# Kernel optimization log

Measured on AMD Instinct MI355X. Metric: run time of the kernel, lower is better.

Reference implementation:

```python
import jax, jax.numpy as jnp
import numpy as np

DIM = 192
NUM_HEADS = 6
WS = 7            # window_size
SS = 3            # shift_size
MLP_HIDDEN = int(DIM * 4.0)
HEAD_DIM = DIM // NUM_HEADS
SCALE = HEAD_DIM ** -0.5
N = WS * WS


def _relative_position_index(ws):
    coords = np.stack(np.meshgrid(np.arange(ws), np.arange(ws), indexing='ij'))  # [2,ws,ws]
    cf = coords.reshape(2, -1)
    rel = cf[:, :, None] - cf[:, None, :]          # [2,N,N]
    rel = rel.transpose(1, 2, 0).copy()
    rel[:, :, 0] += ws - 1
    rel[:, :, 1] += ws - 1
    rel[:, :, 0] *= 2 * ws - 1
    return rel.sum(-1)                              # [N,N]

RPI = jnp.asarray(_relative_position_index(WS))


def _attn_mask(Hp, Wp, ws, ss):
    img = np.zeros((Hp, Wp))
    cnt = 0
    slices = (slice(0, -ws), slice(-ws, -ss), slice(-ss, None))
    for h in slices:
        for w in slices:
            img[h, w] = cnt
            cnt += 1
    mw = img.reshape(Hp // ws, ws, Wp // ws, ws).transpose(0, 2, 1, 3).reshape(-1, ws * ws)
    am = mw[:, None, :] - mw[:, :, None]            # [nWins,N,N]
    am = np.where(am != 0, -100.0, 0.0).astype(np.float32)
    return jnp.asarray(am)


def _layernorm(x, g, b, eps=1e-5):
    mu = jnp.mean(x, axis=-1, keepdims=True)
    var = jnp.mean(jnp.square(x - mu), axis=-1, keepdims=True)
    return (x - mu) * jax.lax.rsqrt(var + eps) * g + b


def setup_inputs() -> dict:
    key = jax.random.key(0)
    ks = jax.random.split(key, 16)
    s = lambda k, shp, sc=0.02: jax.random.normal(k, shp, jnp.float32) * sc
    return {
        'x': jax.random.normal(ks[0], (32, 3136, DIM), jnp.float32),
        'qkv_w': s(ks[1], (DIM, 3 * DIM)),
        'qkv_b': jnp.zeros((3 * DIM,), jnp.float32),
        'proj_w': s(ks[2], (DIM, DIM)),
        'proj_b': jnp.zeros((DIM,), jnp.float32),
        'rpb_table': s(ks[3], ((2 * WS - 1) * (2 * WS - 1), NUM_HEADS)),
        'ln1_g': jnp.ones((DIM,), jnp.float32),
        'ln1_b': jnp.zeros((DIM,), jnp.float32),
        'ln2_g': jnp.ones((DIM,), jnp.float32),
        'ln2_b': jnp.zeros((DIM,), jnp.float32),
        'w1': s(ks[4], (DIM, MLP_HIDDEN)),
        'b1': jnp.zeros((MLP_HIDDEN,), jnp.float32),
        'w2': s(ks[5], (MLP_HIDDEN, DIM)),
        'b2': jnp.zeros((DIM,), jnp.float32),
        'H': 56,
        'W': 56,
    }


def reference(x, qkv_w, qkv_b, proj_w, proj_b, rpb_table, ln1_g, ln1_b,
              ln2_g, ln2_b, w1, b1, w2, b2, H, W):
    B, L, C = x.shape
    shortcut = x
    h = _layernorm(x, ln1_g, ln1_b).reshape(B, H, W, C)

    pad_r = (WS - W % WS) % WS
    pad_b = (WS - H % WS) % WS
    h = jnp.pad(h, ((0, 0), (0, pad_b), (0, pad_r), (0, 0)))
    Hp, Wp = H + pad_b, W + pad_r
    nH, nW = Hp // WS, Wp // WS
    nWins = nH * nW

    if SS > 0:
        h = jnp.roll(h, shift=(-SS, -SS), axis=(1, 2))
        attn_mask = _attn_mask(Hp, Wp, WS, SS)       # [nWins,N,N]
    else:
        attn_mask = None

    # window partition -> [B*nWins, N, C]
    win = h.reshape(B, nH, WS, nW, WS, C).transpose(0, 1, 3, 2, 4, 5)
    win = win.reshape(B * nWins, N, C)

    # attention
    qkv = win @ qkv_w + qkv_b                        # [B_,N,3C]
    qkv = qkv.reshape(-1, N, 3, NUM_HEADS, HEAD_DIM).transpose(2, 0, 3, 1, 4)
    q, k, v = qkv[0] * SCALE, qkv[1], qkv[2]         # [B_,h,N,d]
    attn = jnp.einsum('bhnd,bhmd->bhnm', q, k)

    rpb = rpb_table[RPI.reshape(-1)].reshape(N, N, NUM_HEADS).transpose(2, 0, 1)
    attn = attn + rpb[None]
    if attn_mask is not None:
        attn = attn.reshape(B, nWins, NUM_HEADS, N, N) + attn_mask[None, :, None]
        attn = attn.reshape(-1, NUM_HEADS, N, N)
    attn = jax.nn.softmax(attn, axis=-1)
    out = jnp.einsum('bhnm,bhmd->bhnd', attn, v).transpose(0, 2, 1, 3).reshape(-1, N, C)
    out = out @ proj_w + proj_b

    # window reverse
    out = out.reshape(B, nH, nW, WS, WS, C).transpose(0, 1, 3, 2, 4, 5).reshape(B, Hp, Wp, C)
    if SS > 0:
        out = jnp.roll(out, shift=(SS, SS), axis=(1, 2))
    if pad_r > 0 or pad_b > 0:
        out = out[:, :H, :W, :]
    out = out.reshape(B, H * W, C)

    h = shortcut + out
    ff = _layernorm(h, ln2_g, ln2_b)
    ff = jax.nn.gelu(ff @ w1 + b1, approximate=False) @ w2 + b2
    return h + ff
```

## Files before the change

### kernel.cpp

```cpp
#include <hip/hip_runtime.h>
#include <hip/hip_bf16.h>
#include <cstdint>

typedef __hip_bfloat16 bf16;
typedef __attribute__((ext_vector_type(4))) float f32x4;
typedef __attribute__((ext_vector_type(8))) __bf16 bf16x8;

#define SCALE 0.17677669529663687f

#define OFF_WTQ   0
#define OFF_WTP   221184
#define OFF_WT1   294912
#define OFF_WT2   589824
#define OFF_RMAP  884736
#define OFF_A     1286144
#define OFF_B     39821312
#define OFF_C     193961984

__global__ __launch_bounds__(256) void prep_k(
    const float* __restrict__ qkv_w, const float* __restrict__ proj_w,
    const float* __restrict__ w1, const float* __restrict__ w2,
    bf16* __restrict__ wtq, bf16* __restrict__ wtp,
    bf16* __restrict__ wt1, bf16* __restrict__ wt2, int* __restrict__ rmap)
{
  int i = blockIdx.x * 256 + threadIdx.x;
  if (i < 110592) {
    int n = i / 192, k = i - n * 192;
    wtq[i] = __float2bfloat16(qkv_w[k * 576 + n]);
  } else if (i < 147456) {
    int j = i - 110592; int n = j / 192, k = j - n * 192;
    wtp[j] = __float2bfloat16(proj_w[k * 192 + n]);
  } else if (i < 294912) {
    int j = i - 147456; int n = j / 192, k = j - n * 192;
    wt1[j] = __float2bfloat16(w1[k * 768 + n]);
  } else if (i < 442368) {
    int j = i - 294912; int n = j / 768, k = j - n * 768;
    wt2[j] = __float2bfloat16(w2[k * 192 + n]);
  } else if (i < 542720) {
    int m = i - 442368;
    int win = m / 49, nn = m - win * 49;
    int b = win >> 6, iw = win & 63;
    int wh = iw >> 3, ww = iw & 7;
    int ty = nn / 7, tx = nn - ty * 7;
    int rr = wh * 7 + ty + 3; if (rr >= 56) rr -= 56;
    int cc = ww * 7 + tx + 3; if (cc >= 56) cc -= 56;
    rmap[m] = b * 3136 + rr * 56 + cc;
  }
}

template<bool MAP>
__global__ __launch_bounds__(256) void ln_k(
    const float* __restrict__ x, const float* __restrict__ g,
    const float* __restrict__ b, const int* __restrict__ rmap,
    bf16* __restrict__ out)
{
  int wv = threadIdx.x >> 6, lane = threadIdx.x & 63;
  long m = (long)blockIdx.x * 4 + wv;
  long src = MAP ? (long)rmap[m] : m;
  const float* row = x + src * 192;
  float v0 = row[lane], v1 = row[lane + 64], v2 = row[lane + 128];
  float s = v0 + v1 + v2;
  #pragma unroll
  for (int d = 1; d < 64; d <<= 1) s += __shfl_xor(s, d, 64);
  float mu = s * (1.0f / 192.0f);
  float d0 = v0 - mu, d1 = v1 - mu, d2 = v2 - mu;
  float q = d0 * d0 + d1 * d1 + d2 * d2;
  #pragma unroll
  for (int d = 1; d < 64; d <<= 1) q += __shfl_xor(q, d, 64);
  float inv = 1.0f / sqrtf(q * (1.0f / 192.0f) + 1e-5f);
  bf16* o = out + m * 192;
  o[lane]       = __float2bfloat16(d0 * inv * g[lane]       + b[lane]);
  o[lane + 64]  = __float2bfloat16(d1 * inv * g[lane + 64]  + b[lane + 64]);
  o[lane + 128] = __float2bfloat16(d2 * inv * g[lane + 128] + b[lane + 128]);
}

template<int MODE, int KD>
__global__ __launch_bounds__(256) void gemm_k(
    const bf16* __restrict__ A, const bf16* __restrict__ Bt,
    const float* __restrict__ bias, const float* __restrict__ extra,
    const int* __restrict__ rmap, void* __restrict__ outp)
{
  __shared__ bf16 As[128 * 64];
  const int tid = threadIdx.x;
  const int lane = tid & 63;
  const int w = tid >> 6;
  const int wm = w >> 1, wn = w & 1;
  const long m0 = (long)blockIdx.y * 128;
  const int n0 = blockIdx.x * 64;
  const int r = lane & 15, kb = lane >> 4;

  f32x4 acc[4][2];
  #pragma unroll
  for (int a = 0; a < 4; ++a)
    #pragma unroll
    for (int bb = 0; bb < 2; ++bb) acc[a][bb] = (f32x4){0.f, 0.f, 0.f, 0.f};

  for (int k0 = 0; k0 < KD; k0 += 64) {
    #pragma unroll
    for (int it = 0; it < 4; ++it) {
      int li = tid + it * 256;
      int m = li >> 3;
      int sl = (li & 7) ^ (m & 7);
      const bf16* src = A + (m0 + m) * KD + k0 + sl * 8;
      bf16* dst = As + (size_t)(w * 64 + it * 256) * 8;
      __builtin_amdgcn_global_load_lds(
          (const __attribute__((address_space(1))) unsigned int*)src,
          (__attribute__((address_space(3))) unsigned int*)dst, 16, 0, 0);
    }
    __syncthreads();

    bf16x8 af[2][4], bfr[2][2];
    #pragma unroll
    for (int h2 = 0; h2 < 2; ++h2) {
      #pragma unroll
      for (int mi = 0; mi < 4; ++mi) {
        int m = wm * 64 + mi * 16 + r;
        int slot = (h2 * 4 + kb) ^ (r & 7);
        af[h2][mi] = *(const bf16x8*)(As + m * 64 + slot * 8);
      }
      #pragma unroll
      for (int ni = 0; ni < 2; ++ni) {
        int n = n0 + wn * 32 + ni * 16 + r;
        bfr[h2][ni] = *(const bf16x8*)(Bt + (long)n * KD + k0 + h2 * 32 + kb * 8);
      }
    }
    #pragma unroll
    for (int h2 = 0; h2 < 2; ++h2)
      #pragma unroll
      for (int mi = 0; mi < 4; ++mi)
        #pragma unroll
        for (int ni = 0; ni < 2; ++ni)
          acc[mi][ni] = __builtin_amdgcn_mfma_f32_16x16x32_bf16(
              af[h2][mi], bfr[h2][ni], acc[mi][ni], 0, 0, 0);
    __syncthreads();
  }

  #pragma unroll
  for (int mi = 0; mi < 4; ++mi) {
    #pragma unroll
    for (int ni = 0; ni < 2; ++ni) {
      int col = n0 + wn * 32 + ni * 16 + r;
      float bb = bias[col];
      #pragma unroll
      for (int rr = 0; rr < 4; ++rr) {
        long row = m0 + wm * 64 + mi * 16 + kb * 4 + rr;
        float c = acc[mi][ni][rr] + bb;
        if constexpr (MODE == 0) {
          ((bf16*)outp)[row * 576 + col] = __float2bfloat16(c);
        } else {
          long gr = rmap[row];
          ((float*)outp)[gr * 192 + col] = extra[gr * 192 + col] + c;
        }
      }
    }
  }
}

#define ALS 200
#define W1S 200
#define HLS 72
#define W2S 72
__global__ __launch_bounds__(512) void mlp_k(
    const float* __restrict__ h, const float* __restrict__ g2,
    const float* __restrict__ bg2, const bf16* __restrict__ w1t,
    const float* __restrict__ b1, const bf16* __restrict__ w2t,
    const float* __restrict__ b2, float* __restrict__ outp)
{
  __shared__ bf16 Al[128 * ALS];
  __shared__ bf16 W1c[64 * W1S];
  __shared__ bf16 Hl[128 * HLS];
  __shared__ bf16 W2c[192 * W2S];
  const int tid = threadIdx.x;
  const int lane = tid & 63, w = tid >> 6;
  const int wm = w >> 1, wn = w & 1;
  const int r = lane & 15, kb = lane >> 4;
  const long m0 = (long)blockIdx.x * 128;

  bf16x8 wst[6];
  #pragma unroll
  for (int j = 0; j < 3; ++j) {
    int uu = j * 512 + tid;
    int row = uu / 24, sl = uu - row * 24;
    wst[j] = *(const bf16x8*)(w1t + row * 192 + sl * 8);
  }
  #pragma unroll
  for (int j = 0; j < 3; ++j) {
    int uu = j * 512 + tid;
    int row = uu >> 3, sl = uu & 7;
    wst[3 + j] = *(const bf16x8*)(w2t + row * 768 + sl * 8);
  }

  {
    float gv0 = g2[lane], gv1 = g2[lane + 64], gv2 = g2[lane + 128];
    float bv0 = bg2[lane], bv1 = bg2[lane + 64], bv2 = bg2[lane + 128];
    #pragma unroll
    for (int half = 0; half < 2; ++half) {
      float va[8][3];
      #pragma unroll
      for (int i = 0; i < 8; ++i) {
        const float* row = h + (m0 + w * 16 + half * 8 + i) * 192;
        va[i][0] = row[lane]; va[i][1] = row[lane + 64]; va[i][2] = row[lane + 128];
      }
      #pragma unroll
      for (int i = 0; i < 8; ++i) {
        float s = va[i][0] + va[i][1] + va[i][2];
        #pragma unroll
        for (int d = 1; d < 64; d <<= 1) s += __shfl_xor(s, d, 64);
        float mu = s * (1.0f / 192.0f);
        float d0 = va[i][0] - mu, d1 = va[i][1] - mu, d2 = va[i][2] - mu;
        float q = d0 * d0 + d1 * d1 + d2 * d2;
        #pragma unroll
        for (int d = 1; d < 64; d <<= 1) q += __shfl_xor(q, d, 64);
        float inv = 1.0f / sqrtf(q * (1.0f / 192.0f) + 1e-5f);
        bf16* o = Al + (w * 16 + half * 8 + i) * ALS;
        o[lane]       = __float2bfloat16(d0 * inv * gv0 + bv0);
        o[lane + 64]  = __float2bfloat16(d1 * inv * gv1 + bv1);
        o[lane + 128] = __float2bfloat16(d2 * inv * gv2 + bv2);
      }
    }
  }

  #pragma unroll
  for (int j = 0; j < 3; ++j) {
    int uu = j * 512 + tid;
    int row = uu / 24, sl = uu - row * 24;
    *(bf16x8*)(W1c + row * W1S + sl * 8) = wst[j];
    int row2 = uu >> 3, sl2 = uu & 7;
    *(bf16x8*)(W2c + row2 * W2S + sl2 * 8) = wst[3 + j];
  }
  __syncthreads();

  bf16x8 af[2][6];
  #pragma unroll
  for (int mi = 0; mi < 2; ++mi)
    #pragma unroll
    for (int ks = 0; ks < 6; ++ks)
      af[mi][ks] = *(const bf16x8*)(Al + (wm * 32 + mi * 16 + r) * ALS + ks * 32 + kb * 8);

  f32x4 oacc[2][6];
  #pragma unroll
  for (int mi = 0; mi < 2; ++mi)
    #pragma unroll
    for (int nj = 0; nj < 6; ++nj) oacc[mi][nj] = (f32x4){0.f, 0.f, 0.f, 0.f};

  for (int c = 0; c < 12; ++c) {
    f32x4 hacc[2][2];
    #pragma unroll
    for (int mi = 0; mi < 2; ++mi)
      #pragma unroll
      for (int nj = 0; nj < 2; ++nj) hacc[mi][nj] = (f32x4){0.f, 0.f, 0.f, 0.f};
    #pragma unroll
    for (int ks = 0; ks < 6; ++ks) {
      bf16x8 bfr[2];
      #pragma unroll
      for (int nj = 0; nj < 2; ++nj)
        bfr[nj] = *(const bf16x8*)(W1c + (wn * 32 + nj * 16 + r) * W1S + ks * 32 + kb * 8);
      #pragma unroll
      for (int mi = 0; mi < 2; ++mi)
        #pragma unroll
        for (int nj = 0; nj < 2; ++nj)
          hacc[mi][nj] = __builtin_amdgcn_mfma_f32_16x16x32_bf16(af[mi][ks], bfr[nj], hacc[mi][nj], 0, 0, 0);
    }
    #pragma unroll
    for (int nj = 0; nj < 2; ++nj) {
      float b1v = b1[c * 64 + wn * 32 + nj * 16 + r];
      #pragma unroll
      for (int mi = 0; mi < 2; ++mi) {
        #pragma unroll
        for (int rr = 0; rr < 4; ++rr) {
          float xv = hacc[mi][nj][rr] + b1v;
          float t = __expf(fmaf(0.0713548162f * xv, xv * xv, 1.5957692f * xv));
          float ge = xv * t / (t + 1.0f);
          Hl[(wm * 32 + mi * 16 + kb * 4 + rr) * HLS + wn * 32 + nj * 16 + r] = __float2bfloat16(ge);
        }
      }
    }
    if (c + 1 < 12) {
      #pragma unroll
      for (int j = 0; j < 3; ++j) {
        int uu = j * 512 + tid;
        int row = uu / 24, sl = uu - row * 24;
        wst[j] = *(const bf16x8*)(w1t + ((c + 1) * 64 + row) * 192 + sl * 8);
      }
      #pragma unroll
      for (int j = 0; j < 3; ++j) {
        int uu = j * 512 + tid;
        int row = uu >> 3, sl = uu & 7;
        wst[3 + j] = *(const bf16x8*)(w2t + row * 768 + (c + 1) * 64 + sl * 8);
      }
    }
    __syncthreads();

    #pragma unroll
    for (int ks = 0; ks < 2; ++ks) {
      bf16x8 ha[2], wb[6];
      #pragma unroll
      for (int mi = 0; mi < 2; ++mi)
        ha[mi] = *(const bf16x8*)(Hl + (wm * 32 + mi * 16 + r) * HLS + ks * 32 + kb * 8);
      #pragma unroll
      for (int nj = 0; nj < 6; ++nj)
        wb[nj] = *(const bf16x8*)(W2c + (wn * 96 + nj * 16 + r) * W2S + ks * 32 + kb * 8);
      #pragma unroll
      for (int mi = 0; mi < 2; ++mi)
        #pragma unroll
        for (int nj = 0; nj < 6; ++nj)
          oacc[mi][nj] = __builtin_amdgcn_mfma_f32_16x16x32_bf16(ha[mi], wb[nj], oacc[mi][nj], 0, 0, 0);
    }
    __syncthreads();

    if (c + 1 < 12) {
      #pragma unroll
      for (int j = 0; j < 3; ++j) {
        int uu = j * 512 + tid;
        int row = uu / 24, sl = uu - row * 24;
        *(bf16x8*)(W1c + row * W1S + sl * 8) = wst[j];
        int row2 = uu >> 3, sl2 = uu & 7;
        *(bf16x8*)(W2c + row2 * W2S + sl2 * 8) = wst[3 + j];
      }
      __syncthreads();
    }
  }

  #pragma unroll
  for (int mi = 0; mi < 2; ++mi) {
    #pragma unroll
    for (int nj = 0; nj < 6; ++nj) {
      int col = wn * 96 + nj * 16 + r;
      float b2v = b2[col];
      #pragma unroll
      for (int rr = 0; rr < 4; ++rr) {
        long row = m0 + wm * 32 + mi * 16 + kb * 4 + rr;
        outp[row * 192 + col] = h[row * 192 + col] + oacc[mi][nj][rr] + b2v;
      }
    }
  }
}

__global__ __launch_bounds__(64) void attn_k(
    const bf16* __restrict__ qkv, const float* __restrict__ rpb,
    bf16* __restrict__ aout)
{
  __shared__ bf16 P[64 * 72];
  __shared__ bf16 Vt[32 * 72];
  int lane = threadIdx.x;
  int r = lane & 15, kb = lane >> 4;
  int head = blockIdx.x % 6;
  int win = blockIdx.x / 6;
  int iw = win & 63;
  int wh = iw >> 3, ww = iw & 7;
  const bf16* base = qkv + (long)win * (49 * 576);

  bf16x8 qf[4], kf[4];
  #pragma unroll
  for (int t = 0; t < 4; ++t) {
    int row = t * 16 + r;
    if (row < 49) {
      qf[t] = *(const bf16x8*)(base + row * 576 + head * 32 + kb * 8);
      kf[t] = *(const bf16x8*)(base + row * 576 + 192 + head * 32 + kb * 8);
    } else {
      qf[t] = (bf16x8){0, 0, 0, 0, 0, 0, 0, 0};
      kf[t] = (bf16x8){0, 0, 0, 0, 0, 0, 0, 0};
    }
  }
  f32x4 zero = {0.f, 0.f, 0.f, 0.f};
  f32x4 s[4][4];
  #pragma unroll
  for (int ti = 0; ti < 4; ++ti)
    #pragma unroll
    for (int tj = 0; tj < 4; ++tj)
      s[ti][tj] = __builtin_amdgcn_mfma_f32_16x16x32_bf16(qf[ti], kf[tj], zero, 0, 0, 0);

  {
    int j = lane;
    if (j < 49) {
      #pragma unroll
      for (int d0 = 0; d0 < 32; d0 += 8) {
        bf16x8 v8 = *(const bf16x8*)(base + j * 576 + 384 + head * 32 + d0);
        #pragma unroll
        for (int u = 0; u < 8; ++u) Vt[(d0 + u) * 72 + j] = *((const bf16*)&v8 + u);
      }
    } else {
      for (int d = 0; d < 32; ++d) Vt[d * 72 + j] = __float2bfloat16(0.0f);
    }
  }

  #pragma unroll
  for (int ti = 0; ti < 4; ++ti) {
    #pragma unroll
    for (int rr = 0; rr < 4; ++rr) {
      int i = ti * 16 + kb * 4 + rr;
      int ii = i < 49 ? i : 48;
      int yi = ii / 7, xi = ii - yi * 7;
      int ari = wh * 7 + yi, aci = ww * 7 + xi;
      int gi = (ari < 49 ? 0 : (ari < 53 ? 1 : 2)) * 3 + (aci < 49 ? 0 : (aci < 53 ? 1 : 2));
      float vals[4];
      #pragma unroll
      for (int tj = 0; tj < 4; ++tj) {
        int j = tj * 16 + r;
        int jj = j < 49 ? j : 48;
        int yj = jj / 7, xj = jj - yj * 7;
        float pb = rpb[((yi - yj + 6) * 13 + (xi - xj + 6)) * 6 + head];
        int arj = wh * 7 + yj, acj = ww * 7 + xj;
        int gj = (arj < 49 ? 0 : (arj < 53 ? 1 : 2)) * 3 + (acj < 49 ? 0 : (acj < 53 ? 1 : 2));
        float v = s[ti][tj][rr] * SCALE + pb;
        if (gi != gj) v -= 100.0f;
        if (i >= 49 || j >= 49) v = -1e30f;
        vals[tj] = v;
      }
      float mx = fmaxf(fmaxf(vals[0], vals[1]), fmaxf(vals[2], vals[3]));
      #pragma unroll
      for (int d = 1; d < 16; d <<= 1) mx = fmaxf(mx, __shfl_xor(mx, d, 64));
      float e0 = __expf(vals[0] - mx), e1 = __expf(vals[1] - mx);
      float e2 = __expf(vals[2] - mx), e3 = __expf(vals[3] - mx);
      float sum = e0 + e1 + e2 + e3;
      #pragma unroll
      for (int d = 1; d < 16; d <<= 1) sum += __shfl_xor(sum, d, 64);
      float inv = 1.0f / sum;
      P[i * 72 + 0  + r] = __float2bfloat16(e0 * inv);
      P[i * 72 + 16 + r] = __float2bfloat16(e1 * inv);
      P[i * 72 + 32 + r] = __float2bfloat16(e2 * inv);
      P[i * 72 + 48 + r] = __float2bfloat16(e3 * inv);
    }
  }
  __syncthreads();

  f32x4 o[4][2];
  #pragma unroll
  for (int ti = 0; ti < 4; ++ti)
    #pragma unroll
    for (int dt = 0; dt < 2; ++dt) o[ti][dt] = zero;
  #pragma unroll
  for (int kt = 0; kt < 2; ++kt) {
    bf16x8 pf[4], vf[2];
    #pragma unroll
    for (int ti = 0; ti < 4; ++ti)
      pf[ti] = *(const bf16x8*)(P + (ti * 16 + r) * 72 + kt * 32 + kb * 8);
    #pragma unroll
    for (int dt = 0; dt < 2; ++dt)
      vf[dt] = *(const bf16x8*)(Vt + (dt * 16 + r) * 72 + kt * 32 + kb * 8);
    #pragma unroll
    for (int ti = 0; ti < 4; ++ti)
      #pragma unroll
      for (int dt = 0; dt < 2; ++dt)
        o[ti][dt] = __builtin_amdgcn_mfma_f32_16x16x32_bf16(pf[ti], vf[dt], o[ti][dt], 0, 0, 0);
  }
  #pragma unroll
  for (int ti = 0; ti < 4; ++ti)
    #pragma unroll
    for (int dt = 0; dt < 2; ++dt)
      #pragma unroll
      for (int rr = 0; rr < 4; ++rr) {
        int i = ti * 16 + kb * 4 + rr;
        if (i < 49)
          aout[((long)win * 49 + i) * 192 + head * 32 + dt * 16 + r] =
              __float2bfloat16(o[ti][dt][rr]);
      }
}

extern "C" void kernel_launch(void* const* d_in, const int* in_sizes, int n_in,
                              void* d_out, int out_size, void* d_ws, size_t ws_size,
                              hipStream_t stream)
{
  const float* x      = (const float*)d_in[0];
  const float* qkv_w  = (const float*)d_in[1];
  const float* qkv_b  = (const float*)d_in[2];
  const float* proj_w = (const float*)d_in[3];
  const float* proj_b = (const float*)d_in[4];
  const float* rpb    = (const float*)d_in[5];
  const float* ln1_g  = (const float*)d_in[6];
  const float* ln1_b  = (const float*)d_in[7];
  const float* ln2_g  = (const float*)d_in[8];
  const float* ln2_b  = (const float*)d_in[9];
  const float* w1     = (const float*)d_in[10];
  const float* b1     = (const float*)d_in[11];
  const float* w2     = (const float*)d_in[12];
  const float* b2     = (const float*)d_in[13];

  char* ws = (char*)d_ws;
  bf16* wtq = (bf16*)(ws + OFF_WTQ);
  bf16* wtp = (bf16*)(ws + OFF_WTP);
  bf16* wt1 = (bf16*)(ws + OFF_WT1);
  bf16* wt2 = (bf16*)(ws + OFF_WT2);
  int*  rmap = (int*)(ws + OFF_RMAP);
  bf16* Abuf = (bf16*)(ws + OFF_A);
  bf16* Bbuf = (bf16*)(ws + OFF_B);
  float* hbuf = (float*)(ws + OFF_C);

  prep_k<<<2120, 256, 0, stream>>>(qkv_w, proj_w, w1, w2, wtq, wtp, wt1, wt2, rmap);
  ln_k<true><<<25088, 256, 0, stream>>>(x, ln1_g, ln1_b, rmap, Abuf);
  gemm_k<0, 192><<<dim3(9, 784), 256, 0, stream>>>(Abuf, wtq, qkv_b, nullptr, nullptr, Bbuf);
  attn_k<<<12288, 64, 0, stream>>>(Bbuf, rpb, Abuf);
  gemm_k<1, 192><<<dim3(3, 784), 256, 0, stream>>>(Abuf, wtp, proj_b, x, rmap, hbuf);
  mlp_k<<<784, 512, 0, stream>>>(hbuf, ln2_g, ln2_b, wt1, b1, wt2, b2, (float*)d_out);
}
```

Before: 527.0 us.

## Restructure fused MLP kernel with swizzled LDS, double-buffered weights, 2x4 warp grid

The fused LN2+MLP kernel drops padded LDS strides in favour of XOR-swizzled layouts. It double-buffers the W1/W2 chunk tiles so each iteration needs one fewer barrier, and changes the warp grid from 4x2 to 2x4 so each warp holds 64 rows and reuses one B fragment across four M tiles. The aim is to cut LDS bank conflicts and barrier stalls and to raise MFMA density per LDS load. The cost is more A-fragment registers (af[4][6]) and larger shared memory (112KB), with launch bounds asking for 2 blocks per CU, which may not fit.

```diff
diff --git a/kernel.cpp b/kernel.cpp
--- a/kernel.cpp
+++ b/kernel.cpp
@@ -156,23 +156,18 @@
   }
 }
 
-#define ALS 200
-#define W1S 200
-#define HLS 72
-#define W2S 72
-__global__ __launch_bounds__(512) void mlp_k(
+__global__ __launch_bounds__(512, 2) void mlp_k(
     const float* __restrict__ h, const float* __restrict__ g2,
     const float* __restrict__ bg2, const bf16* __restrict__ w1t,
     const float* __restrict__ b1, const bf16* __restrict__ w2t,
     const float* __restrict__ b2, float* __restrict__ outp)
 {
-  __shared__ bf16 Al[128 * ALS];
-  __shared__ bf16 W1c[64 * W1S];
-  __shared__ bf16 Hl[128 * HLS];
-  __shared__ bf16 W2c[192 * W2S];
+  __shared__ __align__(16) char smem[114688];
+  bf16* const Al = (bf16*)smem;
+  bf16* const Hl = (bf16*)(smem + 98304);
   const int tid = threadIdx.x;
   const int lane = tid & 63, w = tid >> 6;
-  const int wm = w >> 1, wn = w & 1;
+  const int wm2 = w >> 2, wn4 = w & 3;
   const int r = lane & 15, kb = lane >> 4;
   const long m0 = (long)blockIdx.x * 128;
 
@@ -182,17 +177,14 @@
     int uu = j * 512 + tid;
     int row = uu / 24, sl = uu - row * 24;
     wst[j] = *(const bf16x8*)(w1t + row * 192 + sl * 8);
-  }
-  #pragma unroll
-  for (int j = 0; j < 3; ++j) {
-    int uu = j * 512 + tid;
-    int row = uu >> 3, sl = uu & 7;
-    wst[3 + j] = *(const bf16x8*)(w2t + row * 768 + sl * 8);
+    int row2 = uu >> 3, sl2 = uu & 7;
+    wst[3 + j] = *(const bf16x8*)(w2t + row2 * 768 + sl2 * 8);
   }
 
   {
     float gv0 = g2[lane], gv1 = g2[lane + 64], gv2 = g2[lane + 128];
     float bv0 = bg2[lane], bv1 = bg2[lane + 64], bv2 = bg2[lane + 128];
+    int u0 = lane >> 3, cl = lane & 7;
     #pragma unroll
     for (int half = 0; half < 2; ++half) {
       float va[8][3];
@@ -203,6 +195,7 @@
       }
       #pragma unroll
       for (int i = 0; i < 8; ++i) {
+        int rowi = w * 16 + half * 8 + i;
         float s = va[i][0] + va[i][1] + va[i][2];
         #pragma unroll
         for (int d = 1; d < 64; d <<= 1) s += __shfl_xor(s, d, 64);
@@ -212,67 +205,60 @@
         #pragma unroll
         for (int d = 1; d < 64; d <<= 1) q += __shfl_xor(q, d, 64);
         float inv = 1.0f / sqrtf(q * (1.0f / 192.0f) + 1e-5f);
-        bf16* o = Al + (w * 16 + half * 8 + i) * ALS;
-        o[lane]       = __float2bfloat16(d0 * inv * gv0 + bv0);
-        o[lane + 64]  = __float2bfloat16(d1 * inv * gv1 + bv1);
-        o[lane + 128] = __float2bfloat16(d2 * inv * gv2 + bv2);
-      }
-    }
-  }
-
-  #pragma unroll
-  for (int j = 0; j < 3; ++j) {
-    int uu = j * 512 + tid;
-    int row = uu / 24, sl = uu - row * 24;
-    *(bf16x8*)(W1c + row * W1S + sl * 8) = wst[j];
-    int row2 = uu >> 3, sl2 = uu & 7;
-    *(bf16x8*)(W2c + row2 * W2S + sl2 * 8) = wst[3 + j];
+        bf16* o = Al + rowi * 192;
+        int rx = rowi & 7;
+        o[((u0 ^ rx) << 3) + cl]              = __float2bfloat16(d0 * inv * gv0 + bv0);
+        o[((8 | ((u0 ^ rx) & 7)) << 3) + cl]  = __float2bfloat16(d1 * inv * gv1 + bv1);
+        o[((16 | ((u0 ^ rx) & 7)) << 3) + cl] = __float2bfloat16(d2 * inv * gv2 + bv2);
+      }
+    }
+  }
+
+  {
+    bf16* W1c = (bf16*)(smem + 49152);
+    bf16* W2c = (bf16*)(smem + 73728);
+    #pragma unroll
+    for (int j = 0; j < 3; ++j) {
+      int uu = j * 512 + tid;
+      int row = uu / 24, u = uu - row * 24;
+      int up = (u & ~7) | ((u ^ row) & 7);
+      *(bf16x8*)(W1c + row * 192 + up * 8) = wst[j];
+      int row2 = uu >> 3, u2 = uu & 7;
+      *(bf16x8*)(W2c + row2 * 64 + ((u2 ^ (row2 & 7)) << 3)) = wst[3 + j];
+    }
   }
   __syncthreads();
 
-  bf16x8 af[2][6];
-  #pragma unroll
-  for (int mi = 0; mi < 2; ++mi)
-    #pragma unroll
-    for (int ks = 0; ks < 6; ++ks)
-      af[mi][ks] = *(const bf16x8*)(Al + (wm * 32 + mi * 16 + r) * ALS + ks * 32 + kb * 8);
-
-  f32x4 oacc[2][6];
-  #pragma unroll
-  for (int mi = 0; mi < 2; ++mi)
-    #pragma unroll
-    for (int nj = 0; nj < 6; ++nj) oacc[mi][nj] = (f32x4){0.f, 0.f, 0.f, 0.f};
+  bf16x8 af[4][6];
+  #pragma unroll
+  for (int mt = 0; mt < 4; ++mt) {
+    int row = wm2 * 64 + mt * 16 + r;
+    #pragma unroll
+    for (int ks = 0; ks < 6; ++ks) {
+      int u = ks * 4 + kb;
+      int up = (u & ~7) | ((u ^ row) & 7);
+      af[mt][ks] = *(const bf16x8*)(Al + row * 192 + up * 8);
+    }
+  }
+
+  f32x4 oacc[4][3];
+  #pragma unroll
+  for (int mt = 0; mt < 4; ++mt)
+    #pragma unroll
+    for (int nt = 0; nt < 3; ++nt) oacc[mt][nt] = (f32x4){0.f, 0.f, 0.f, 0.f};
 
   for (int c = 0; c < 12; ++c) {
-    f32x4 hacc[2][2];
-    #pragma unroll
-    for (int mi = 0; mi < 2; ++mi)
-      #pragma unroll
-      for (int nj = 0; nj < 2; ++nj) hacc[mi][nj] = (f32x4){0.f, 0.f, 0.f, 0.f};
-    #pragma unroll
-    for (int ks = 0; ks < 6; ++ks) {
-      bf16x8 bfr[2];
-      #pragma unroll
-      for (int nj = 0; nj < 2; ++nj)
-        bfr[nj] = *(const bf16x8*)(W1c + (wn * 32 + nj * 16 + r) * W1S + ks * 32 + kb * 8);
-      #pragma unroll
-      for (int mi = 0; mi < 2; ++mi)
-        #pragma unroll
-        for (int nj = 0; nj < 2; ++nj)
-          hacc[mi][nj] = __builtin_amdgcn_mfma_f32_16x16x32_bf16(af[mi][ks], bfr[nj], hacc[mi][nj], 0, 0, 0);
-    }
-    #pragma unroll
-    for (int nj = 0; nj < 2; ++nj) {
-      float b1v = b1[c * 64 + wn * 32 + nj * 16 + r];
-      #pragma unroll
-      for (int mi = 0; mi < 2; ++mi) {
-        #pragma unroll
-        for (int rr = 0; rr < 4; ++rr) {
-          float xv = hacc[mi][nj][rr] + b1v;
-          float t = __expf(fmaf(0.0713548162f * xv, xv * xv, 1.5957692f * xv));
-          float ge = xv * t / (t + 1.0f);
-          Hl[(wm * 32 + mi * 16 + kb * 4 + rr) * HLS + wn * 32 + nj * 16 + r] = __float2bfloat16(ge);
-        }
+    bf16* W1c = (bf16*)(smem + ((c & 1) ? 0 : 49152));
+    bf16* W2c = (bf16*)(smem + ((c & 1) ? 24576 : 73728));
+
+    bf16x8 bfr[6];
+    {
+      int row = wn4 * 16 + r;
+      #pragma unroll
+      for (int ks = 0; ks < 6; ++ks) {
+        int u = ks * 4 + kb;
+        int up = (u & ~7) | ((u ^ row) & 7);
+        bfr[ks] = *(const bf16x8*)(W1c + row * 192 + up * 8);
       }
     }
     if (c + 1 < 12) {
@@ -281,56 +267,80 @@
         int uu = j * 512 + tid;
         int row = uu / 24, sl = uu - row * 24;
         wst[j] = *(const bf16x8*)(w1t + ((c + 1) * 64 + row) * 192 + sl * 8);
-      }
+        int row2 = uu >> 3, sl2 = uu & 7;
+        wst[3 + j] = *(const bf16x8*)(w2t + row2 * 768 + (c + 1) * 64 + sl2 * 8);
+      }
+    }
+    f32x4 hacc[4];
+    #pragma unroll
+    for (int mt = 0; mt < 4; ++mt) hacc[mt] = (f32x4){0.f, 0.f, 0.f, 0.f};
+    #pragma unroll
+    for (int ks = 0; ks < 6; ++ks)
+      #pragma unroll
+      for (int mt = 0; mt < 4; ++mt)
+        hacc[mt] = __builtin_amdgcn_mfma_f32_16x16x32_bf16(af[mt][ks], bfr[ks], hacc[mt], 0, 0, 0);
+    {
+      float b1v = b1[c * 64 + wn4 * 16 + r];
+      #pragma unroll
+      for (int mt = 0; mt < 4; ++mt) {
+        #pragma unroll
+        for (int rr = 0; rr < 4; ++rr) {
+          int row = wm2 * 64 + mt * 16 + kb * 4 + rr;
+          int col = wn4 * 16 + r;
+          float xv = hacc[mt][rr] + b1v;
+          float t = __expf(fmaf(0.0713548162f * xv, xv * xv, 1.5957692f * xv));
+          float ge = xv * t / (t + 1.0f);
+          Hl[row * 64 + (((col >> 3) ^ (row & 7)) << 3) + (col & 7)] = __float2bfloat16(ge);
+        }
+      }
+    }
+    __syncthreads();
+
+    #pragma unroll
+    for (int ks = 0; ks < 2; ++ks) {
+      bf16x8 ha[4], wb[3];
+      #pragma unroll
+      for (int mt = 0; mt < 4; ++mt) {
+        int row = wm2 * 64 + mt * 16 + r;
+        ha[mt] = *(const bf16x8*)(Hl + row * 64 + (((ks * 4 + kb) ^ (row & 7)) << 3));
+      }
+      #pragma unroll
+      for (int nt = 0; nt < 3; ++nt) {
+        int n = wn4 * 48 + nt * 16 + r;
+        wb[nt] = *(const bf16x8*)(W2c + n * 64 + (((ks * 4 + kb) ^ (n & 7)) << 3));
+      }
+      #pragma unroll
+      for (int mt = 0; mt < 4; ++mt)
+        #pragma unroll
+        for (int nt = 0; nt < 3; ++nt)
+          oacc[mt][nt] = __builtin_amdgcn_mfma_f32_16x16x32_bf16(ha[mt], wb[nt], oacc[mt][nt], 0, 0, 0);
+    }
+    if (c + 1 < 12) {
+      bf16* nW1 = (bf16*)(smem + ((c & 1) ? 49152 : 0));
+      bf16* nW2 = (bf16*)(smem + ((c & 1) ? 73728 : 24576));
       #pragma unroll
       for (int j = 0; j < 3; ++j) {
         int uu = j * 512 + tid;
-        int row = uu >> 3, sl = uu & 7;
-        wst[3 + j] = *(const bf16x8*)(w2t + row * 768 + (c + 1) * 64 + sl * 8);
+        int row = uu / 24, u = uu - row * 24;
+        int up = (u & ~7) | ((u ^ row) & 7);
+        *(bf16x8*)(nW1 + row * 192 + up * 8) = wst[j];
+        int row2 = uu >> 3, u2 = uu & 7;
+        *(bf16x8*)(nW2 + row2 * 64 + ((u2 ^ (row2 & 7)) << 3)) = wst[3 + j];
       }
     }
     __syncthreads();
-
-    #pragma unroll
-    for (int ks = 0; ks < 2; ++ks) {
-      bf16x8 ha[2], wb[6];
-      #pragma unroll
-      for (int mi = 0; mi < 2; ++mi)
-        ha[mi] = *(const bf16x8*)(Hl + (wm * 32 + mi * 16 + r) * HLS + ks * 32 + kb * 8);
-      #pragma unroll
-      for (int nj = 0; nj < 6; ++nj)
-        wb[nj] = *(const bf16x8*)(W2c + (wn * 96 + nj * 16 + r) * W2S + ks * 32 + kb * 8);
-      #pragma unroll
-      for (int mi = 0; mi < 2; ++mi)
-        #pragma unroll
-        for (int nj = 0; nj < 6; ++nj)
-          oacc[mi][nj] = __builtin_amdgcn_mfma_f32_16x16x32_bf16(ha[mi], wb[nj], oacc[mi][nj], 0, 0, 0);
-    }
-    __syncthreads();
-
-    if (c + 1 < 12) {
-      #pragma unroll
-      for (int j = 0; j < 3; ++j) {
-        int uu = j * 512 + tid;
-        int row = uu / 24, sl = uu - row * 24;
-        *(bf16x8*)(W1c + row * W1S + sl * 8) = wst[j];
-        int row2 = uu >> 3, sl2 = uu & 7;
-        *(bf16x8*)(W2c + row2 * W2S + sl2 * 8) = wst[3 + j];
-      }
-      __syncthreads();
-    }
-  }
-
-  #pragma unroll
-  for (int mi = 0; mi < 2; ++mi) {
-    #pragma unroll
-    for (int nj = 0; nj < 6; ++nj) {
-      int col = wn * 96 + nj * 16 + r;
+  }
+
+  #pragma unroll
+  for (int mt = 0; mt < 4; ++mt) {
+    #pragma unroll
+    for (int nt = 0; nt < 3; ++nt) {
+      int col = wn4 * 48 + nt * 16 + r;
       float b2v = b2[col];
       #pragma unroll
       for (int rr = 0; rr < 4; ++rr) {
-        long row = m0 + wm * 32 + mi * 16 + kb * 4 + rr;
-        outp[row * 192 + col] = h[row * 192 + col] + oacc[mi][nj][rr] + b2v;
+        long row = m0 + wm2 * 64 + mt * 16 + kb * 4 + rr;
+        outp[row * 192 + col] = h[row * 192 + col] + oacc[mt][nt][rr] + b2v;
       }
     }
   }
```

After: 524.5 us. No clear change (-0.5%).
